# Kernel optimization log

Hardware: AMD Instinct MI355X
Metric: run time of the kernel (lower is better)

## Reference

```python
import jax, jax.numpy as jnp
import numpy as np

B, CI, CO = 16, 16, 16
M1, M2, M3 = 6, 6, 6
NT, NX, NY = 39, 28, 28
NXr, NYr = 14, 14  # int((n-1)/2 + 1) for n=28


def setup_inputs() -> dict:
    key = jax.random.key(0)
    ks = jax.random.split(key, 9)
    scale = 1.0 / (CI * CO)
    u = lambda k, s: scale * jax.random.uniform(k, s, dtype=jnp.float32)
    return {
        "x": jax.random.normal(ks[0], (B, CI, NT, NXr, NYr), dtype=jnp.float32),
        "wp1_re": u(ks[1], (CI, CO, M1)), "wp1_im": u(ks[2], (CI, CO, M1)),
        "wp2_re": u(ks[3], (CI, CO, M2)), "wp2_im": u(ks[4], (CI, CO, M2)),
        "wp3_re": u(ks[5], (CI, CO, M3)), "wp3_im": u(ks[6], (CI, CO, M3)),
        "wr_re": u(ks[7], (CI, CO, M1, M2, M3)), "wr_im": u(ks[8], (CI, CO, M1, M2, M3)),
    }


def _forward(x, wp1, wp2, wp3, wr):
    # grids (match torch.linspace with hardcoded nt/nx/ny and truncation)
    tt_np = np.linspace(0.0, NT - 1, NT)
    tx_np = np.linspace(0.0, 1.0, NX)[:NXr]
    ty_np = np.linspace(0.0, 1.0, NY)[:NYr]
    dtt = float(tt_np[1] - tt_np[0])
    dtx = float(tx_np[1] - tx_np[0])
    dty = float(ty_np[1] - ty_np[0])

    alpha = jnp.fft.fftn(x, axes=(-3, -2, -1))  # [B, CI, NT, NXr, NYr] complex64

    lam1 = (2j * np.pi * jnp.fft.fftfreq(NT, dtt)).astype(jnp.complex64)   # [NT]
    lam2 = (2j * np.pi * jnp.fft.fftfreq(NXr, dtx)).astype(jnp.complex64)  # [NXr]
    lam3 = (2j * np.pi * jnp.fft.fftfreq(NYr, dty)).astype(jnp.complex64)  # [NYr]

    # per-axis pole reciprocals: 1/((l1-p1)(l2-p2)(l3-p3)) = (1/(l1-p1))(1/(l2-p2))(1/(l3-p3))
    r1 = 1.0 / (lam1[:, None, None, None] - wp1[None])  # [NT,  CI, CO, M1]
    r2 = 1.0 / (lam2[:, None, None, None] - wp2[None])  # [NXr, CI, CO, M2]
    r3 = 1.0 / (lam3[:, None, None, None] - wp3[None])  # [NYr, CI, CO, M3]

    # Hw[m,n,l,i,k,p,q,r] = wr[i,k,p,q,r]*r1[m,i,k,p]*r2[n,i,k,q]*r3[l,i,k,r]
    # output_residue1[b,k,m,n,l] = sum_{i,p,q,r} alpha[b,i,m,n,l] * Hw
    or1 = jnp.einsum('bimnl,ikpqr,mikp,nikq,likr->bkmnl', alpha, wr, r1, r2, r3)
    # output_residue2[b,k,p,q,r] = -sum_{i,m,n,l} alpha[b,i,m,n,l] * Hw
    or2 = -jnp.einsum('bimnl,ikpqr,mikp,nikq,likr->bkpqr', alpha, wr, r1, r2, r3)

    x1 = jnp.real(jnp.fft.ifftn(or1, s=(NT, NXr, NYr), axes=(-3, -2, -1))).astype(jnp.float32)

    tt = jnp.asarray(tt_np, dtype=jnp.float32).astype(jnp.complex64)
    tx = jnp.asarray(tx_np, dtype=jnp.float32).astype(jnp.complex64)
    ty = jnp.asarray(ty_np, dtype=jnp.float32).astype(jnp.complex64)

    e1 = jnp.exp(wp1[..., None] * tt)  # [CI, CO, M1, NT]
    e2 = jnp.exp(wp2[..., None] * tx)  # [CI, CO, M2, NXr]
    e3 = jnp.exp(wp3[..., None] * ty)  # [CI, CO, M3, NYr]

    # x2[k,i,z,x,y] = Re( sum_{b,p,q,m} or2[k,b,p,q,m]*e1[b,i,p,z]*e2[b,i,q,x]*e3[b,i,m,y] )
    x2 = jnp.real(jnp.einsum('kbpqm,bipz,biqx,bimy->kizxy', or2, e1, e2, e3)).astype(jnp.float32)
    x2 = x2 / (NT * NXr * NYr)
    return x1 + x2


def reference(x, wp1_re, wp1_im, wp2_re, wp2_im, wp3_re, wp3_im, wr_re, wr_im):
    wp1 = jax.lax.complex(wp1_re, wp1_im)
    wp2 = jax.lax.complex(wp2_re, wp2_im)
    wp3 = jax.lax.complex(wp3_re, wp3_im)
    wr = jax.lax.complex(wr_re, wr_im)
    return _forward(x, wp1, wp2, wp3, wr)
```

## Files before the change

kernel.cpp:

```cpp
#include <hip/hip_runtime.h>

constexpr int kB  = 16;
constexpr int kC  = 16;
constexpr int kM  = 6;
constexpr int kNT = 39;
constexpr int kNX = 14;
constexpr int kNY = 14;
constexpr int kNS = kNX * kNY;
constexpr int kNF = kNT * kNS;
constexpr int kNIK = kC * kC;
constexpr int kMR = kM * kM * kM;
constexpr int kFCH = 6;

__device__ __forceinline__ float2 cmul(float2 a, float2 b) {
    return make_float2(a.x * b.x - a.y * b.y, a.x * b.y + a.y * b.x);
}
__device__ __forceinline__ void cfma(float2& c, float2 a, float2 b) {
    c.x = fmaf(a.x, b.x, fmaf(-a.y, b.y, c.x));
    c.y = fmaf(a.x, b.y, fmaf(a.y, b.x, c.y));
}

__global__ __launch_bounds__(256) void k_init(
    const float* __restrict__ wp1_re, const float* __restrict__ wp1_im,
    const float* __restrict__ wp2_re, const float* __restrict__ wp2_im,
    const float* __restrict__ wp3_re, const float* __restrict__ wp3_im,
    float2* __restrict__ F39, float2* __restrict__ F14,
    float2* __restrict__ r1t, float2* __restrict__ r2t, float2* __restrict__ r3t,
    float2* __restrict__ e1t, float2* __restrict__ e2t, float2* __restrict__ e3t)
{
    const float PI2 = 6.283185307179586f;
    int tid = blockIdx.x * blockDim.x + threadIdx.x;
    int nth = gridDim.x * blockDim.x;

    for (int idx = tid; idx < kNT * kNT; idx += nth) {
        int m = idx / kNT, t = idx % kNT;
        float ang = -PI2 * (float)((m * t) % kNT) / (float)kNT;
        float s, c; sincosf(ang, &s, &c);
        F39[idx] = make_float2(c, s);
    }
    for (int idx = tid; idx < kNX * kNX; idx += nth) {
        int a = idx / kNX, b = idx % kNX;
        float ang = -PI2 * (float)((a * b) % kNX) / (float)kNX;
        float s, c; sincosf(ang, &s, &c);
        F14[idx] = make_float2(c, s);
    }
    for (int idx = tid; idx < kNIK * kM * kNT; idx += nth) {
        int z = idx % kNT; int ikp = idx / kNT;
        float wre = wp1_re[ikp], wim = wp1_im[ikp];
        float f = (z < 20 ? (float)z : (float)(z - kNT)) / (float)kNT;
        float w = PI2 * f;
        float dr = -wre, di = w - wim;
        float inv = 1.0f / (dr * dr + di * di);
        r1t[idx] = make_float2(dr * inv, -di * inv);
        float tt = (float)z;
        float er = expf(wre * tt);
        float s, c; sincosf(wim * tt, &s, &c);
        e1t[idx] = make_float2(er * c, er * s);
    }
    for (int idx = tid; idx < kNIK * kM * kNX; idx += nth) {
        int n = idx % kNX; int ikq = idx / kNX;
        float f = (n <= 6 ? (float)n : (float)(n - kNX)) * 27.0f / 14.0f;
        float w = PI2 * f;
        float tx = (float)n * (1.0f / 27.0f);
        {
            float wre = wp2_re[ikq], wim = wp2_im[ikq];
            float dr = -wre, di = w - wim;
            float inv = 1.0f / (dr * dr + di * di);
            r2t[idx] = make_float2(dr * inv, -di * inv);
            float er = expf(wre * tx);
            float s, c; sincosf(wim * tx, &s, &c);
            e2t[idx] = make_float2(er * c, er * s);
        }
        {
            float wre = wp3_re[ikq], wim = wp3_im[ikq];
            float dr = -wre, di = w - wim;
            float inv = 1.0f / (dr * dr + di * di);
            r3t[idx] = make_float2(dr * inv, -di * inv);
            float er = expf(wre * tx);
            float s, c; sincosf(wim * tx, &s, &c);
            e3t[idx] = make_float2(er * c, er * s);
        }
    }
}

__global__ __launch_bounds__(256) void k_dft_t_real(
    const float* __restrict__ x, const float2* __restrict__ F39, float2* __restrict__ out)
{
    int bc = blockIdx.x, mg = blockIdx.y;
    __shared__ float2 Fs[13 * kNT];
    int t = threadIdx.x;
    for (int j = t; j < 13 * kNT; j += 256)
        Fs[j] = F39[(mg * 13 + j / kNT) * kNT + (j % kNT)];
    __syncthreads();
    if (t < kNS) {
        float col[kNT];
        const float* xp = x + (size_t)bc * kNF + t;
        #pragma unroll
        for (int tt = 0; tt < kNT; ++tt) col[tt] = xp[(size_t)tt * kNS];
        for (int mi = 0; mi < 13; ++mi) {
            float2 acc = make_float2(0.f, 0.f);
            #pragma unroll
            for (int tt = 0; tt < kNT; ++tt) {
                float2 f = Fs[mi * kNT + tt];
                acc.x = fmaf(f.x, col[tt], acc.x);
                acc.y = fmaf(f.y, col[tt], acc.y);
            }
            out[((size_t)bc * kNT + mg * 13 + mi) * kNS + t] = acc;
        }
    }
}

__global__ __launch_bounds__(256) void k_idft_t(
    const float2* __restrict__ in, const float2* __restrict__ F39, float2* __restrict__ out)
{
    int bk = blockIdx.x, zg = blockIdx.y;
    __shared__ float2 Fs[13 * kNT];
    int t = threadIdx.x;
    for (int j = t; j < 13 * kNT; j += 256) {
        float2 f = F39[(zg * 13 + j / kNT) * kNT + (j % kNT)];
        f.y = -f.y;
        Fs[j] = f;
    }
    __syncthreads();
    if (t < kNS) {
        float2 col[kNT];
        const float2* ip = in + (size_t)bk * kNF + t;
        #pragma unroll
        for (int m = 0; m < kNT; ++m) col[m] = ip[(size_t)m * kNS];
        for (int zi = 0; zi < 13; ++zi) {
            float2 acc = make_float2(0.f, 0.f);
            #pragma unroll
            for (int m = 0; m < kNT; ++m) cfma(acc, Fs[zi * kNT + m], col[m]);
            out[((size_t)bk * kNT + zg * 13 + zi) * kNS + t] = acc;
        }
    }
}

__global__ __launch_bounds__(256) void k_dft_xy(
    const float2* __restrict__ in, const float2* __restrict__ F14, float2* __restrict__ out)
{
    int bm = blockIdx.x;
    __shared__ float2 tile[kNS];
    __shared__ float2 tmp[kNS];
    __shared__ float2 Fs[kNX * kNX];
    int t = threadIdx.x;
    if (t < kNS) tile[t] = in[(size_t)bm * kNS + t];
    if (t < kNX * kNX) Fs[t] = F14[t];
    __syncthreads();
    if (t < kNS) {
        int n2 = t / kNY, l = t % kNY;
        float2 acc = make_float2(0.f, 0.f);
        #pragma unroll
        for (int n = 0; n < kNX; ++n) cfma(acc, Fs[n2 * kNX + n], tile[n * kNY + l]);
        tmp[t] = acc;
    }
    __syncthreads();
    if (t < kNS) {
        int n = t / kNY, l2 = t % kNY;
        float2 acc = make_float2(0.f, 0.f);
        #pragma unroll
        for (int l = 0; l < kNY; ++l) cfma(acc, Fs[l2 * kNY + l], tmp[n * kNY + l]);
        out[(size_t)bm * kNS + t] = acc;
    }
}

__global__ __launch_bounds__(256) void k_idft_xy_final(
    const float2* __restrict__ in, const float2* __restrict__ F14, float* __restrict__ outp)
{
    int bm = blockIdx.x;
    __shared__ float2 tile[kNS];
    __shared__ float2 tmp[kNS];
    __shared__ float2 Fs[kNX * kNX];
    int t = threadIdx.x;
    if (t < kNS) tile[t] = in[(size_t)bm * kNS + t];
    if (t < kNX * kNX) { float2 f = F14[t]; f.y = -f.y; Fs[t] = f; }
    __syncthreads();
    if (t < kNS) {
        int n2 = t / kNY, l = t % kNY;
        float2 acc = make_float2(0.f, 0.f);
        #pragma unroll
        for (int n = 0; n < kNX; ++n) cfma(acc, Fs[n2 * kNX + n], tile[n * kNY + l]);
        tmp[t] = acc;
    }
    __syncthreads();
    if (t < kNS) {
        int n = t / kNY, l2 = t % kNY;
        float2 acc = make_float2(0.f, 0.f);
        #pragma unroll
        for (int l = 0; l < kNY; ++l) cfma(acc, Fs[l2 * kNY + l], tmp[n * kNY + l]);
        outp[(size_t)bm * kNS + t] += acc.x * (1.0f / 7644.0f);
    }
}

__global__ __launch_bounds__(256) void k_H(
    const float* __restrict__ wr_re, const float* __restrict__ wr_im,
    const float2* __restrict__ r1t, const float2* __restrict__ r2t,
    const float2* __restrict__ r3t, float2* __restrict__ H)
{
    int ik = blockIdx.x;
    __shared__ float2 wrs[kMR];
    __shared__ float2 r1s[kM * kNT];
    __shared__ float2 r2s[kM * kNX];
    __shared__ float2 r3s[kM * kNY];
    __shared__ float2 As[kM * kM * kNY];
    __shared__ float2 Ss[kM * kNS];
    int t = threadIdx.x;
    for (int j = t; j < kMR; j += 256)
        wrs[j] = make_float2(wr_re[ik * kMR + j], wr_im[ik * kMR + j]);
    for (int j = t; j < kM * kNT; j += 256) r1s[j] = r1t[(size_t)ik * kM * kNT + j];
    for (int j = t; j < kM * kNX; j += 256) r2s[j] = r2t[(size_t)ik * kM * kNX + j];
    for (int j = t; j < kM * kNY; j += 256) r3s[j] = r3t[(size_t)ik * kM * kNY + j];
    __syncthreads();
    for (int j = t; j < kM * kM * kNY; j += 256) {
        int l = j % kNY; int pq = j / kNY;
        float2 acc = make_float2(0.f, 0.f);
        #pragma unroll
        for (int r = 0; r < kM; ++r) cfma(acc, wrs[pq * kM + r], r3s[r * kNY + l]);
        As[j] = acc;
    }
    __syncthreads();
    for (int j = t; j < kM * kNS; j += 256) {
        int l = j % kNY; int n = (j / kNY) % kNX; int p = j / kNS;
        float2 acc = make_float2(0.f, 0.f);
        #pragma unroll
        for (int q = 0; q < kM; ++q) cfma(acc, r2s[q * kNX + n], As[(p * kM + q) * kNY + l]);
        Ss[j] = acc;
    }
    __syncthreads();
    for (int j = t; j < kNF; j += 256) {
        int m = j / kNS; int nl = j % kNS;
        float2 acc = make_float2(0.f, 0.f);
        #pragma unroll
        for (int p = 0; p < kM; ++p) cfma(acc, r1s[p * kNT + m], Ss[p * kNS + nl]);
        H[(size_t)ik * kNF + j] = acc;
    }
}

__global__ __launch_bounds__(256) void k_or1(
    const float2* __restrict__ alpha, const float2* __restrict__ H, float2* __restrict__ out)
{
    int f0 = blockIdx.x * kFCH;
    __shared__ float2 As[256 * 7 + 16];
    __shared__ float2 Hs[256 * 7 + 16];
    int t = threadIdx.x;
    {
        const float2* ap = alpha + (size_t)t * kNF + f0;
        const float2* hp = H + (size_t)t * kNF + f0;
        int base = t * 7 + (t >> 4);
        #pragma unroll
        for (int j = 0; j < kFCH; ++j) {
            As[base + j] = ap[j];
            Hs[base + j] = hp[j];
        }
    }
    __syncthreads();
    int b = t >> 4, k = t & 15;
    float2 acc[kFCH];
    #pragma unroll
    for (int j = 0; j < kFCH; ++j) acc[j] = make_float2(0.f, 0.f);
    #pragma unroll
    for (int i = 0; i < kC; ++i) {
        int ai = (b * 16 + i) * 7 + b;
        int hi = (i * 16 + k) * 7 + i;
        #pragma unroll
        for (int j = 0; j < kFCH; ++j) cfma(acc[j], As[ai + j], Hs[hi + j]);
    }
    float2* op = out + (size_t)t * kNF + f0;
    #pragma unroll
    for (int j = 0; j < kFCH; ++j) op[j] = acc[j];
}

__global__ __launch_bounds__(256) void k_or2p(
    const float2* __restrict__ alpha,
    const float* __restrict__ wr_re, const float* __restrict__ wr_im,
    const float2* __restrict__ r1t, const float2* __restrict__ r2t,
    const float2* __restrict__ r3t, float2* __restrict__ P)
{
    int blk = blockIdx.x;
    int i = blk % kC; int bk = blk / kC;
    int b = bk / kC, k = bk % kC;
    int ik = i * kC + k;
    __shared__ float2 r1s[kM * kNT];
    __shared__ float2 r2s[kM * kNX];
    __shared__ float2 r3s[kM * kNY];
    __shared__ float2 wrs[kMR];
    __shared__ float2 T1[kM * kNS];
    __shared__ float2 T2[kM * kM * kNY];
    int t = threadIdx.x;
    for (int j = t; j < kM * kNT; j += 256) r1s[j] = r1t[(size_t)ik * kM * kNT + j];
    for (int j = t; j < kM * kNX; j += 256) r2s[j] = r2t[(size_t)ik * kM * kNX + j];
    for (int j = t; j < kM * kNY; j += 256) r3s[j] = r3t[(size_t)ik * kM * kNY + j];
    for (int j = t; j < kMR; j += 256)
        wrs[j] = make_float2(wr_re[ik * kMR + j], wr_im[ik * kMR + j]);
    __syncthreads();
    if (t < kNS) {
        float2 c0 = make_float2(0.f, 0.f), c1 = c0, c2 = c0, c3 = c0, c4 = c0, c5 = c0;
        const float2* ap = alpha + (size_t)(b * kC + i) * kNF + t;
        for (int m = 0; m < kNT; ++m) {
            float2 a = ap[(size_t)m * kNS];
            cfma(c0, a, r1s[0 * kNT + m]);
            cfma(c1, a, r1s[1 * kNT + m]);
            cfma(c2, a, r1s[2 * kNT + m]);
            cfma(c3, a, r1s[3 * kNT + m]);
            cfma(c4, a, r1s[4 * kNT + m]);
            cfma(c5, a, r1s[5 * kNT + m]);
        }
        T1[0 * kNS + t] = c0; T1[1 * kNS + t] = c1; T1[2 * kNS + t] = c2;
        T1[3 * kNS + t] = c3; T1[4 * kNS + t] = c4; T1[5 * kNS + t] = c5;
    }
    __syncthreads();
    for (int j = t; j < kM * kM * kNY; j += 256) {
        int l = j % kNY; int q = (j / kNY) % kM; int p = j / (kNY * kM);
        float2 a2 = make_float2(0.f, 0.f);
        #pragma unroll
        for (int n = 0; n < kNX; ++n) cfma(a2, T1[p * kNS + n * kNY + l], r2s[q * kNX + n]);
        T2[j] = a2;
    }
    __syncthreads();
    if (t < kMR) {
        int r = t % kM; int q = (t / kM) % kM; int p = t / (kM * kM);
        float2 t3 = make_float2(0.f, 0.f);
        #pragma unroll
        for (int l = 0; l < kNY; ++l) cfma(t3, T2[(p * kM + q) * kNY + l], r3s[r * kNY + l]);
        P[(size_t)blk * kMR + t] = cmul(wrs[t], t3);
    }
}

__global__ __launch_bounds__(256) void k_or2red(
    const float2* __restrict__ P, float2* __restrict__ or2)
{
    int id = blockIdx.x * blockDim.x + threadIdx.x;
    if (id >= kB * kC * kMR) return;
    int t = id % kMR; int bk = id / kMR;
    float2 s = make_float2(0.f, 0.f);
    #pragma unroll
    for (int i = 0; i < kC; ++i) {
        float2 v = P[((size_t)bk * kC + i) * kMR + t];
        s.x += v.x; s.y += v.y;
    }
    or2[id] = make_float2(-s.x, -s.y);
}

__global__ __launch_bounds__(256) void k_x2zp(
    const float2* __restrict__ or2,
    const float2* __restrict__ e1t, const float2* __restrict__ e2t,
    const float2* __restrict__ e3t, float* __restrict__ P2)
{
    int bk = blockIdx.x; int b = bk / kC, k = bk % kC;
    int z0 = blockIdx.y * 13;
    int c0 = blockIdx.z * 8;
    __shared__ float2 e1s[kM * kNT];
    __shared__ float2 e2s[kM * kNX];
    __shared__ float2 e3s[kM * kNY];
    __shared__ float2 o2s[kMR];
    __shared__ float2 Us[kM * kM * kNY];
    int t = threadIdx.x;
    int xx = t / kNY, yy = t % kNY;
    float accz[13];
    #pragma unroll
    for (int zi = 0; zi < 13; ++zi) accz[zi] = 0.f;

    for (int ci = 0; ci < 8; ++ci) {
        int c = c0 + ci;
        __syncthreads();
        int ck = c * kC + k;
        for (int j = t; j < kM * kNT; j += 256) e1s[j] = e1t[(size_t)ck * kM * kNT + j];
        for (int j = t; j < kM * kNX; j += 256) e2s[j] = e2t[(size_t)ck * kM * kNX + j];
        for (int j = t; j < kM * kNY; j += 256) e3s[j] = e3t[(size_t)ck * kM * kNY + j];
        for (int j = t; j < kMR; j += 256) o2s[j] = or2[(size_t)(b * kC + c) * kMR + j];
        __syncthreads();
        for (int j = t; j < kM * kM * kNY; j += 256) {
            int y = j % kNY; int pq = j / kNY;
            float2 u = make_float2(0.f, 0.f);
            #pragma unroll
            for (int m = 0; m < kM; ++m) cfma(u, o2s[pq * kM + m], e3s[m * kNY + y]);
            Us[j] = u;
        }
        __syncthreads();
        if (t < kNS) {
            float2 V[kM];
            #pragma unroll
            for (int p = 0; p < kM; ++p) {
                float2 v = make_float2(0.f, 0.f);
                #pragma unroll
                for (int q = 0; q < kM; ++q) cfma(v, Us[(p * kM + q) * kNY + yy], e2s[q * kNX + xx]);
                V[p] = v;
            }
            #pragma unroll
            for (int p = 0; p < kM; ++p) {
                #pragma unroll
                for (int zi = 0; zi < 13; ++zi) {
                    float2 e = e1s[p * kNT + z0 + zi];
                    accz[zi] = fmaf(V[p].x, e.x, accz[zi]);
                    accz[zi] = fmaf(-V[p].y, e.y, accz[zi]);
                }
            }
        }
    }
    if (t < kNS) {
        size_t base = ((size_t)(bk * 2 + blockIdx.z)) * kNF + (size_t)z0 * kNS + t;
        #pragma unroll
        for (int zi = 0; zi < 13; ++zi) P2[base + (size_t)zi * kNS] = accz[zi];
    }
}

__global__ __launch_bounds__(256) void k_x2red(
    const float* __restrict__ P2, float* __restrict__ outp)
{
    int id = blockIdx.x * blockDim.x + threadIdx.x;
    if (id >= kB * kC * kNF) return;
    int f = id % kNF; int bk = id / kNF;
    const float sc = 1.0f / 7644.0f;
    outp[id] = (P2[(size_t)(2 * bk) * kNF + f] + P2[(size_t)(2 * bk + 1) * kNF + f]) * sc;
}

extern "C" void kernel_launch(void* const* d_in, const int* in_sizes, int n_in,
                              void* d_out, int out_size, void* d_ws, size_t ws_size,
                              hipStream_t stream) {
    (void)in_sizes; (void)n_in; (void)out_size; (void)ws_size;
    const float* x      = (const float*)d_in[0];
    const float* wp1_re = (const float*)d_in[1];
    const float* wp1_im = (const float*)d_in[2];
    const float* wp2_re = (const float*)d_in[3];
    const float* wp2_im = (const float*)d_in[4];
    const float* wp3_re = (const float*)d_in[5];
    const float* wp3_im = (const float*)d_in[6];
    const float* wr_re  = (const float*)d_in[7];
    const float* wr_im  = (const float*)d_in[8];
    float* out = (float*)d_out;

    const size_t big = (size_t)kNIK * kNF;
    float2* A   = (float2*)d_ws;
    float2* Bb  = A + big;
    float2* Cc  = Bb + big;
    float2* OR2 = Cc + big;
    float2* r1t = OR2 + (size_t)kB * kC * kMR;
    float2* r2t = r1t + (size_t)kNIK * kM * kNT;
    float2* r3t = r2t + (size_t)kNIK * kM * kNX;
    float2* e1t = r3t + (size_t)kNIK * kM * kNY;
    float2* e2t = e1t + (size_t)kNIK * kM * kNT;
    float2* e3t = e2t + (size_t)kNIK * kM * kNX;
    float2* F39 = e3t + (size_t)kNIK * kM * kNY;
    float2* F14 = F39 + kNT * kNT;

    k_init<<<64, 256, 0, stream>>>(wp1_re, wp1_im, wp2_re, wp2_im, wp3_re, wp3_im,
                                   F39, F14, r1t, r2t, r3t, e1t, e2t, e3t);
    k_dft_t_real<<<dim3(kNIK, 3), 256, 0, stream>>>(x, F39, A);
    k_dft_xy<<<kNIK * kNT, 256, 0, stream>>>(A, F14, Bb);
    k_H<<<kNIK, 256, 0, stream>>>(wr_re, wr_im, r1t, r2t, r3t, Cc);
    k_or1<<<kNF / kFCH, 256, 0, stream>>>(Bb, Cc, A);
    k_or2p<<<kB * kC * kC, 256, 0, stream>>>(Bb, wr_re, wr_im, r1t, r2t, r3t, Cc);
    k_or2red<<<(kB * kC * kMR + 255) / 256, 256, 0, stream>>>(Cc, OR2);
    k_x2zp<<<dim3(kB * kC, 3, 2), 256, 0, stream>>>(OR2, e1t, e2t, e3t, (float*)Bb);
    k_x2red<<<(kB * kC * kNF + 255) / 256, 256, 0, stream>>>((const float*)Bb, out);
    k_idft_t<<<dim3(kB * kC, 3), 256, 0, stream>>>(A, F39, Cc);
    k_idft_xy_final<<<kNIK * kNT, 256, 0, stream>>>(Cc, F14, out);
}
```

Baseline: 225.0 us.

## Process two batches per block in or2 and x2 kernels, drop x2 reduction

k_or2p now handles a pair of batch indices per block, so each r1/r2/r3/wr tile it loads is reused across two alpha slices, and the grid is halved. The x2 kernel also processes two batches per block and loops over all 16 channels instead of splitting them across blockIdx.z. It writes the scaled result straight to the output, which removes the partial-sum buffer and the separate k_x2red pass. Each block gets longer serial work and fewer blocks run, so parallelism drops; the x2 grid falls to 384 blocks on a large GPU.

```diff
diff --git a/kernel.cpp b/kernel.cpp
--- a/kernel.cpp
+++ b/kernel.cpp
@@ -277,15 +277,18 @@
     const float2* __restrict__ r3t, float2* __restrict__ P)
 {
     int blk = blockIdx.x;
-    int i = blk % kC; int bk = blk / kC;
-    int b = bk / kC, k = bk % kC;
+    int i = blk % kC; int rest = blk / kC;
+    int k = rest % kC; int pb = rest / kC;
+    int b0 = 2 * pb, b1 = 2 * pb + 1;
     int ik = i * kC + k;
     __shared__ float2 r1s[kM * kNT];
     __shared__ float2 r2s[kM * kNX];
     __shared__ float2 r3s[kM * kNY];
     __shared__ float2 wrs[kMR];
-    __shared__ float2 T1[kM * kNS];
-    __shared__ float2 T2[kM * kM * kNY];
+    __shared__ float2 T1a[kM * kNS];
+    __shared__ float2 T1b[kM * kNS];
+    __shared__ float2 T2a[kM * kM * kNY];
+    __shared__ float2 T2b[kM * kM * kNY];
     int t = threadIdx.x;
     for (int j = t; j < kM * kNT; j += 256) r1s[j] = r1t[(size_t)ik * kM * kNT + j];
     for (int j = t; j < kM * kNX; j += 256) r2s[j] = r2t[(size_t)ik * kM * kNX + j];
@@ -295,34 +298,53 @@
     __syncthreads();
     if (t < kNS) {
         float2 c0 = make_float2(0.f, 0.f), c1 = c0, c2 = c0, c3 = c0, c4 = c0, c5 = c0;
-        const float2* ap = alpha + (size_t)(b * kC + i) * kNF + t;
+        float2 d0 = c0, d1 = c0, d2 = c0, d3 = c0, d4 = c0, d5 = c0;
+        const float2* ap0 = alpha + (size_t)(b0 * kC + i) * kNF + t;
+        const float2* ap1 = alpha + (size_t)(b1 * kC + i) * kNF + t;
         for (int m = 0; m < kNT; ++m) {
-            float2 a = ap[(size_t)m * kNS];
-            cfma(c0, a, r1s[0 * kNT + m]);
-            cfma(c1, a, r1s[1 * kNT + m]);
-            cfma(c2, a, r1s[2 * kNT + m]);
-            cfma(c3, a, r1s[3 * kNT + m]);
-            cfma(c4, a, r1s[4 * kNT + m]);
-            cfma(c5, a, r1s[5 * kNT + m]);
-        }
-        T1[0 * kNS + t] = c0; T1[1 * kNS + t] = c1; T1[2 * kNS + t] = c2;
-        T1[3 * kNS + t] = c3; T1[4 * kNS + t] = c4; T1[5 * kNS + t] = c5;
+            float2 a0 = ap0[(size_t)m * kNS];
+            float2 a1 = ap1[(size_t)m * kNS];
+            float2 r;
+            r = r1s[0 * kNT + m]; cfma(c0, a0, r); cfma(d0, a1, r);
+            r = r1s[1 * kNT + m]; cfma(c1, a0, r); cfma(d1, a1, r);
+            r = r1s[2 * kNT + m]; cfma(c2, a0, r); cfma(d2, a1, r);
+            r = r1s[3 * kNT + m]; cfma(c3, a0, r); cfma(d3, a1, r);
+            r = r1s[4 * kNT + m]; cfma(c4, a0, r); cfma(d4, a1, r);
+            r = r1s[5 * kNT + m]; cfma(c5, a0, r); cfma(d5, a1, r);
+        }
+        T1a[0 * kNS + t] = c0; T1a[1 * kNS + t] = c1; T1a[2 * kNS + t] = c2;
+        T1a[3 * kNS + t] = c3; T1a[4 * kNS + t] = c4; T1a[5 * kNS + t] = c5;
+        T1b[0 * kNS + t] = d0; T1b[1 * kNS + t] = d1; T1b[2 * kNS + t] = d2;
+        T1b[3 * kNS + t] = d3; T1b[4 * kNS + t] = d4; T1b[5 * kNS + t] = d5;
     }
     __syncthreads();
     for (int j = t; j < kM * kM * kNY; j += 256) {
         int l = j % kNY; int q = (j / kNY) % kM; int p = j / (kNY * kM);
         float2 a2 = make_float2(0.f, 0.f);
-        #pragma unroll
-        for (int n = 0; n < kNX; ++n) cfma(a2, T1[p * kNS + n * kNY + l], r2s[q * kNX + n]);
-        T2[j] = a2;
+        float2 b2 = make_float2(0.f, 0.f);
+        #pragma unroll
+        for (int n = 0; n < kNX; ++n) {
+            float2 r = r2s[q * kNX + n];
+            cfma(a2, T1a[p * kNS + n * kNY + l], r);
+            cfma(b2, T1b[p * kNS + n * kNY + l], r);
+        }
+        T2a[j] = a2;
+        T2b[j] = b2;
     }
     __syncthreads();
     if (t < kMR) {
         int r = t % kM; int q = (t / kM) % kM; int p = t / (kM * kM);
-        float2 t3 = make_float2(0.f, 0.f);
-        #pragma unroll
-        for (int l = 0; l < kNY; ++l) cfma(t3, T2[(p * kM + q) * kNY + l], r3s[r * kNY + l]);
-        P[(size_t)blk * kMR + t] = cmul(wrs[t], t3);
+        float2 t3a = make_float2(0.f, 0.f);
+        float2 t3b = make_float2(0.f, 0.f);
+        #pragma unroll
+        for (int l = 0; l < kNY; ++l) {
+            float2 rr = r3s[r * kNY + l];
+            cfma(t3a, T2a[(p * kM + q) * kNY + l], rr);
+            cfma(t3b, T2b[(p * kM + q) * kNY + l], rr);
+        }
+        float2 w = wrs[t];
+        P[((size_t)(b0 * kC + k) * kC + i) * kMR + t] = cmul(w, t3a);
+        P[((size_t)(b1 * kC + k) * kC + i) * kMR + t] = cmul(w, t3b);
     }
 }
 
@@ -341,77 +363,91 @@
     or2[id] = make_float2(-s.x, -s.y);
 }
 
-__global__ __launch_bounds__(256) void k_x2zp(
+__global__ __launch_bounds__(256) void k_x2bp(
     const float2* __restrict__ or2,
     const float2* __restrict__ e1t, const float2* __restrict__ e2t,
-    const float2* __restrict__ e3t, float* __restrict__ P2)
-{
-    int bk = blockIdx.x; int b = bk / kC, k = bk % kC;
+    const float2* __restrict__ e3t, float* __restrict__ outp)
+{
+    int bx = blockIdx.x;
+    int k = bx & 15, pb = bx >> 4;
+    int b0 = 2 * pb, b1 = 2 * pb + 1;
     int z0 = blockIdx.y * 13;
-    int c0 = blockIdx.z * 8;
-    __shared__ float2 e1s[kM * kNT];
-    __shared__ float2 e2s[kM * kNX];
+    __shared__ float2 e1s[kM * 13];
+    __shared__ float2 e2s[kNX * kM];
     __shared__ float2 e3s[kM * kNY];
-    __shared__ float2 o2s[kMR];
-    __shared__ float2 Us[kM * kM * kNY];
+    __shared__ float2 o2s0[kMR];
+    __shared__ float2 o2s1[kMR];
+    __shared__ float2 Us0[kM * kM * kNY];
+    __shared__ float2 Us1[kM * kM * kNY];
     int t = threadIdx.x;
     int xx = t / kNY, yy = t % kNY;
-    float accz[13];
+    float accz0[13], accz1[13];
     #pragma unroll
-    for (int zi = 0; zi < 13; ++zi) accz[zi] = 0.f;
-
-    for (int ci = 0; ci < 8; ++ci) {
-        int c = c0 + ci;
+    for (int zi = 0; zi < 13; ++zi) { accz0[zi] = 0.f; accz1[zi] = 0.f; }
+
+    for (int c = 0; c < kC; ++c) {
         __syncthreads();
         int ck = c * kC + k;
-        for (int j = t; j < kM * kNT; j += 256) e1s[j] = e1t[(size_t)ck * kM * kNT + j];
-        for (int j = t; j < kM * kNX; j += 256) e2s[j] = e2t[(size_t)ck * kM * kNX + j];
-        for (int j = t; j < kM * kNY; j += 256) e3s[j] = e3t[(size_t)ck * kM * kNY + j];
-        for (int j = t; j < kMR; j += 256) o2s[j] = or2[(size_t)(b * kC + c) * kMR + j];
+        if (t < kM * 13) {
+            int p = t / 13, zi = t % 13;
+            e1s[t] = e1t[(size_t)ck * (kM * kNT) + p * kNT + z0 + zi];
+        }
+        if (t < kNX * kM) {
+            int x = t / kM, q = t % kM;
+            e2s[t] = e2t[(size_t)ck * (kM * kNX) + q * kNX + x];
+        }
+        if (t < kM * kNY) e3s[t] = e3t[(size_t)ck * (kM * kNY) + t];
+        if (t < kMR) {
+            o2s0[t] = or2[(size_t)(b0 * kC + c) * kMR + t];
+            o2s1[t] = or2[(size_t)(b1 * kC + c) * kMR + t];
+        }
         __syncthreads();
         for (int j = t; j < kM * kM * kNY; j += 256) {
             int y = j % kNY; int pq = j / kNY;
-            float2 u = make_float2(0.f, 0.f);
+            float2 u0 = make_float2(0.f, 0.f);
+            float2 u1 = make_float2(0.f, 0.f);
             #pragma unroll
-            for (int m = 0; m < kM; ++m) cfma(u, o2s[pq * kM + m], e3s[m * kNY + y]);
-            Us[j] = u;
+            for (int m = 0; m < kM; ++m) {
+                float2 e = e3s[m * kNY + y];
+                cfma(u0, o2s0[pq * kM + m], e);
+                cfma(u1, o2s1[pq * kM + m], e);
+            }
+            Us0[j] = u0;
+            Us1[j] = u1;
         }
         __syncthreads();
         if (t < kNS) {
-            float2 V[kM];
+            float2 e2r[kM];
+            #pragma unroll
+            for (int q = 0; q < kM; ++q) e2r[q] = e2s[xx * kM + q];
             #pragma unroll
             for (int p = 0; p < kM; ++p) {
-                float2 v = make_float2(0.f, 0.f);
+                float2 v0 = make_float2(0.f, 0.f);
+                float2 v1 = make_float2(0.f, 0.f);
                 #pragma unroll
-                for (int q = 0; q < kM; ++q) cfma(v, Us[(p * kM + q) * kNY + yy], e2s[q * kNX + xx]);
-                V[p] = v;
-            }
-            #pragma unroll
-            for (int p = 0; p < kM; ++p) {
+                for (int q = 0; q < kM; ++q) {
+                    cfma(v0, Us0[(p * kM + q) * kNY + yy], e2r[q]);
+                    cfma(v1, Us1[(p * kM + q) * kNY + yy], e2r[q]);
+                }
                 #pragma unroll
                 for (int zi = 0; zi < 13; ++zi) {
-                    float2 e = e1s[p * kNT + z0 + zi];
-                    accz[zi] = fmaf(V[p].x, e.x, accz[zi]);
-                    accz[zi] = fmaf(-V[p].y, e.y, accz[zi]);
+                    float2 e = e1s[p * 13 + zi];
+                    accz0[zi] = fmaf(v0.x, e.x, fmaf(-v0.y, e.y, accz0[zi]));
+                    accz1[zi] = fmaf(v1.x, e.x, fmaf(-v1.y, e.y, accz1[zi]));
                 }
             }
         }
     }
     if (t < kNS) {
-        size_t base = ((size_t)(bk * 2 + blockIdx.z)) * kNF + (size_t)z0 * kNS + t;
-        #pragma unroll
-        for (int zi = 0; zi < 13; ++zi) P2[base + (size_t)zi * kNS] = accz[zi];
-    }
-}
-
-__global__ __launch_bounds__(256) void k_x2red(
-    const float* __restrict__ P2, float* __restrict__ outp)
-{
-    int id = blockIdx.x * blockDim.x + threadIdx.x;
-    if (id >= kB * kC * kNF) return;
-    int f = id % kNF; int bk = id / kNF;
-    const float sc = 1.0f / 7644.0f;
-    outp[id] = (P2[(size_t)(2 * bk) * kNF + f] + P2[(size_t)(2 * bk + 1) * kNF + f]) * sc;
+        const float sc = 1.0f / 7644.0f;
+        size_t base0 = ((size_t)(b0 * kC + k) * kNT + z0) * kNS + t;
+        size_t base1 = ((size_t)(b1 * kC + k) * kNT + z0) * kNS + t;
+        #pragma unroll
+        for (int zi = 0; zi < 13; ++zi) {
+            outp[base0 + (size_t)zi * kNS] = accz0[zi] * sc;
+            outp[base1 + (size_t)zi * kNS] = accz1[zi] * sc;
+        }
+    }
 }
 
 extern "C" void kernel_launch(void* const* d_in, const int* in_sizes, int n_in,
@@ -449,10 +485,9 @@
     k_dft_xy<<<kNIK * kNT, 256, 0, stream>>>(A, F14, Bb);
     k_H<<<kNIK, 256, 0, stream>>>(wr_re, wr_im, r1t, r2t, r3t, Cc);
     k_or1<<<kNF / kFCH, 256, 0, stream>>>(Bb, Cc, A);
-    k_or2p<<<kB * kC * kC, 256, 0, stream>>>(Bb, wr_re, wr_im, r1t, r2t, r3t, Cc);
+    k_or2p<<<(kB / 2) * kC * kC, 256, 0, stream>>>(Bb, wr_re, wr_im, r1t, r2t, r3t, Cc);
     k_or2red<<<(kB * kC * kMR + 255) / 256, 256, 0, stream>>>(Cc, OR2);
-    k_x2zp<<<dim3(kB * kC, 3, 2), 256, 0, stream>>>(OR2, e1t, e2t, e3t, (float*)Bb);
-    k_x2red<<<(kB * kC * kNF + 255) / 256, 256, 0, stream>>>((const float*)Bb, out);
+    k_x2bp<<<dim3((kB / 2) * kC, 3), 256, 0, stream>>>(OR2, e1t, e2t, e3t, out);
     k_idft_t<<<dim3(kB * kC, 3), 256, 0, stream>>>(A, F39, Cc);
     k_idft_xy_final<<<kNIK * kNT, 256, 0, stream>>>(Cc, F14, out);
 }
```

Result: faster. 207.6 us (-7.7%).
